# Optimization experiments

Hardware: AMD Instinct MI355X
Metric: run time of the kernel (lower is better)

Reference implementation:

```python
import jax, jax.numpy as jnp
import numpy as np

H = 128
NH = 8  # num attention heads


def _ln(x, g, b, eps=1e-5):
    m = x.mean(-1, keepdims=True)
    v = ((x - m) ** 2).mean(-1, keepdims=True)
    return (x - m) / jnp.sqrt(v + eps) * g + b


def _mha(q_in, kv_in, Wqkv, bqkv, Wo, bo):
    # torch nn.MultiheadAttention with packed in_proj, batch=1, eval (no dropout)
    h = q_in.shape[-1]
    hd = h // NH
    Wq, Wk, Wv = Wqkv[:h], Wqkv[h:2 * h], Wqkv[2 * h:]
    bq, bk, bv = bqkv[:h], bqkv[h:2 * h], bqkv[2 * h:]
    q = (q_in @ Wq.T + bq).reshape(-1, NH, hd).transpose(1, 0, 2)   # [nh, Nq, hd]
    k = (kv_in @ Wk.T + bk).reshape(-1, NH, hd).transpose(1, 0, 2)  # [nh, Nk, hd]
    v = (kv_in @ Wv.T + bv).reshape(-1, NH, hd).transpose(1, 0, 2)
    scores = jnp.einsum('hqd,hkd->hqk', q, k) / jnp.sqrt(jnp.asarray(hd, q.dtype))
    attn = jax.nn.softmax(scores, axis=-1)
    out = jnp.einsum('hqk,hkd->hqd', attn, v)                       # [nh, Nq, hd]
    out = out.transpose(1, 0, 2).reshape(-1, h)
    return out @ Wo.T + bo


def setup_inputs() -> dict:
    key = jax.random.key(0)
    ks = jax.random.split(key, 32)
    s = 0.05
    d = {
        'ligand_features': jax.random.normal(ks[0], (512, 128), jnp.float32),
        'pocket_features': jax.random.normal(ks[1], (1024, 128), jnp.float32),
        'ligand_coords': jax.random.uniform(ks[2], (512, 3), jnp.float32) * 20.0,
        'pocket_coords': jax.random.uniform(ks[3], (1024, 3), jnp.float32) * 20.0,
        # projections
        'Wl': jax.random.normal(ks[4], (H, 128), jnp.float32) * s,
        'bl': jnp.zeros((H,), jnp.float32),
        'Wp': jax.random.normal(ks[5], (H, 128), jnp.float32) * s,
        'bp': jnp.zeros((H,), jnp.float32),
        # distance encoder: 1 -> h/4 -> h/2 -> h
        'Wd1': jax.random.normal(ks[6], (H // 4, 1), jnp.float32) * s,
        'bd1': jnp.zeros((H // 4,), jnp.float32),
        'Wd2': jax.random.normal(ks[7], (H // 2, H // 4), jnp.float32) * s,
        'bd2': jnp.zeros((H // 2,), jnp.float32),
        'Wd3': jax.random.normal(ks[8], (H, H // 2), jnp.float32) * s,
        'bd3': jnp.zeros((H,), jnp.float32),
        # gates
        'Wgl': jax.random.normal(ks[9], (H, 2 * H), jnp.float32) * s,
        'bgl': jnp.zeros((H,), jnp.float32),
        'Wgp': jax.random.normal(ks[10], (H, 2 * H), jnp.float32) * s,
        'bgp': jnp.zeros((H,), jnp.float32),
        # shared cross-attention (packed qkv like torch)
        'Wqkv': jax.random.normal(ks[11], (3 * H, H), jnp.float32) * s,
        'bqkv': jnp.zeros((3 * H,), jnp.float32),
        'Wo': jax.random.normal(ks[12], (H, H), jnp.float32) * s,
        'bo': jnp.zeros((H,), jnp.float32),
        # layer norms
        'g_l': jnp.ones((H,), jnp.float32),
        'be_l': jnp.zeros((H,), jnp.float32),
        'g_p': jnp.ones((H,), jnp.float32),
        'be_p': jnp.zeros((H,), jnp.float32),
    }
    return d


def reference(ligand_features, pocket_features, ligand_coords, pocket_coords,
              Wl, bl, Wp, bp, Wd1, bd1, Wd2, bd2, Wd3, bd3,
              Wgl, bgl, Wgp, bgp, Wqkv, bqkv, Wo, bo,
              g_l, be_l, g_p, be_p):
    lig = ligand_features @ Wl.T + bl   # [Nl, H]
    poc = pocket_features @ Wp.T + bp   # [Np, H]

    # pairwise distances [Nl, Np]
    diff = ligand_coords[:, None, :] - pocket_coords[None, :, :]
    dist = jnp.sqrt(jnp.sum(diff * diff, axis=-1))

    # distance encoder MLP applied elementwise -> [Nl, Np, H]
    e = jax.nn.relu(dist[..., None] @ Wd1.T + bd1)
    e = jax.nn.relu(e @ Wd2.T + bd2)
    enc = e @ Wd3.T + bd3
    m = enc.mean(axis=-1)               # [Nl, Np]

    # ligand enhancement: softmax over pocket axis
    sw_l = jax.nn.softmax(-m, axis=-1)          # [Nl, Np]
    agg_l = sw_l @ poc                          # [Nl, H]
    gate_l = jax.nn.sigmoid(jnp.concatenate([lig, agg_l], axis=-1) @ Wgl.T + bgl)
    lig_enh = gate_l * lig + (1.0 - gate_l) * agg_l

    # pocket enhancement: transposed encoding, softmax over ligand axis
    sw_p = jax.nn.softmax(-m.T, axis=-1)        # [Np, Nl]
    agg_p = sw_p @ lig                          # [Np, H]
    gate_p = jax.nn.sigmoid(jnp.concatenate([poc, agg_p], axis=-1) @ Wgp.T + bgp)
    poc_enh = gate_p * poc + (1.0 - gate_p) * agg_p

    lig_att = _mha(lig_enh, poc_enh, Wqkv, bqkv, Wo, bo)
    poc_att = _mha(poc_enh, lig_enh, Wqkv, bqkv, Wo, bo)

    lig_fused = _ln(lig_enh + lig_att, g_l, be_l)
    poc_fused = _ln(poc_enh + poc_att, g_p, be_p)
    return (lig_fused, poc_fused)
```

## Files before the change

### kernel.cpp

```cpp
#include <hip/hip_runtime.h>
#include <math.h>

#define NL 512
#define NP 1024
#define HDIM 128

#define TAB_N 8192
#define DMAX 34.65f

#define WD3M_OFF 0
#define M_OFF    128
#define LIG_OFF  (M_OFF + NL*NP)
#define POC_OFF  (LIG_OFF + NL*HDIM)
#define LENH_OFF (POC_OFF + NP*HDIM)
#define PENH_OFF (LENH_OFF + NL*HDIM)
#define QKVL_OFF (PENH_OFF + NP*HDIM)
#define QKVP_OFF (QKVL_OFF + NL*384)
#define PARTL_OFF (QKVP_OFF + NP*384)
#define PARTP_OFF (PARTL_OFF + 512*8*8*18)
#define TAB_OFF  QKVL_OFF

__device__ __forceinline__ float dot4f(float4 a, float4 b){
  return fmaf(a.x,b.x, fmaf(a.y,b.y, fmaf(a.z,b.z, a.w*b.w)));
}

__global__ __launch_bounds__(128) void prep_kernel(const float* __restrict__ Wd3,
                                                   const float* __restrict__ bd3,
                                                   float* __restrict__ wsw){
  int t = threadIdx.x;
  if (t < 64){
    float s = 0.f;
    #pragma unroll 8
    for (int i = 0; i < 128; i++) s += Wd3[i*64 + t];
    wsw[t] = s * (1.f/128.f);
  } else if (t == 64){
    float s = 0.f;
    for (int i = 0; i < 128; i++) s += bd3[i];
    wsw[64] = s * (1.f/128.f);
  }
}

__global__ __launch_bounds__(128) void proj_kernel(const float* __restrict__ lf, const float* __restrict__ pf,
                                                   const float* __restrict__ Wl, const float* __restrict__ bl,
                                                   const float* __restrict__ Wp, const float* __restrict__ bp,
                                                   float* __restrict__ lig, float* __restrict__ poc){
  int t = threadIdx.x;
  int row0 = blockIdx.x * 4;
  const float* in; const float* W; const float* bias; float* out;
  if (row0 < NL){ in = lf + (size_t)row0*HDIM; W = Wl; bias = bl; out = lig + (size_t)row0*HDIM; }
  else { int r = row0 - NL; in = pf + (size_t)r*HDIM; W = Wp; bias = bp; out = poc + (size_t)r*HDIM; }
  __shared__ float sin[4*HDIM];
  for (int idx = t; idx < 4*HDIM; idx += 128) sin[idx] = in[idx];
  __syncthreads();
  float bv = bias[t];
  float a0 = bv, a1 = bv, a2 = bv, a3 = bv;
  const float4* wr = (const float4*)(W + (size_t)t*HDIM);
  const float4* s0 = (const float4*)(sin);
  const float4* s1 = (const float4*)(sin + HDIM);
  const float4* s2 = (const float4*)(sin + 2*HDIM);
  const float4* s3 = (const float4*)(sin + 3*HDIM);
  #pragma unroll 8
  for (int k = 0; k < 32; k++){
    float4 w = wr[k];
    a0 = fmaf(w.x, s0[k].x, fmaf(w.y, s0[k].y, fmaf(w.z, s0[k].z, fmaf(w.w, s0[k].w, a0))));
    a1 = fmaf(w.x, s1[k].x, fmaf(w.y, s1[k].y, fmaf(w.z, s1[k].z, fmaf(w.w, s1[k].w, a1))));
    a2 = fmaf(w.x, s2[k].x, fmaf(w.y, s2[k].y, fmaf(w.z, s2[k].z, fmaf(w.w, s2[k].w, a2))));
    a3 = fmaf(w.x, s3[k].x, fmaf(w.y, s3[k].y, fmaf(w.z, s3[k].z, fmaf(w.w, s3[k].w, a3))));
  }
  out[t] = a0; out[HDIM + t] = a1; out[2*HDIM + t] = a2; out[3*HDIM + t] = a3;
}

__global__ __launch_bounds__(256) void table_kernel(const float* __restrict__ Wd1, const float* __restrict__ bd1,
                                                    const float* __restrict__ Wd2, const float* __restrict__ bd2,
                                                    const float* __restrict__ wsw, float* __restrict__ tab){
  __shared__ float sWd1[32], sbd1[32], sWd2[2048], sbd2[64], swd3m[64];
  __shared__ float sbd3m;
  int t = threadIdx.x;
  int idx = blockIdx.x * 256 + t;
  if (t < 32){ sWd1[t] = Wd1[t]; sbd1[t] = bd1[t]; }
  if (t >= 32 && t < 96){ sbd2[t-32] = bd2[t-32]; swd3m[t-32] = wsw[t-32]; }
  if (t == 96) sbd3m = wsw[64];
  for (int k = t; k < 2048; k += 256) sWd2[k] = Wd2[k];
  __syncthreads();

  float d = (float)idx * (DMAX / (float)(TAB_N - 1));

  float4 e1q[8];
  const float4* w1q = (const float4*)sWd1;
  const float4* b1q = (const float4*)sbd1;
  #pragma unroll
  for (int k4 = 0; k4 < 8; k4++){
    float4 w = w1q[k4], b = b1q[k4];
    float4 e;
    e.x = fmaxf(fmaf(d, w.x, b.x), 0.f);
    e.y = fmaxf(fmaf(d, w.y, b.y), 0.f);
    e.z = fmaxf(fmaf(d, w.z, b.z), 0.f);
    e.w = fmaxf(fmaf(d, w.w, b.w), 0.f);
    e1q[k4] = e;
  }
  float mv = sbd3m;
  #pragma unroll 4
  for (int j2 = 0; j2 < 64; j2++){
    const float4* wrow = (const float4*)(sWd2 + j2*32);
    float a0 = 0.f, a1 = 0.f, a2 = 0.f, a3 = 0.f;
    #pragma unroll
    for (int k4 = 0; k4 < 8; k4++){
      float4 w = wrow[k4], e = e1q[k4];
      a0 = fmaf(w.x, e.x, a0);
      a1 = fmaf(w.y, e.y, a1);
      a2 = fmaf(w.z, e.z, a2);
      a3 = fmaf(w.w, e.w, a3);
    }
    float e2v = fmaxf(sbd2[j2] + ((a0+a1)+(a2+a3)), 0.f);
    mv = fmaf(swd3m[j2], e2v, mv);
  }
  tab[idx] = mv;
}

__global__ __launch_bounds__(1024) void agg_gate_fused(const float* __restrict__ lc, const float* __restrict__ pc,
                                                       const float* __restrict__ tab,
                                                       const float* __restrict__ lig, const float* __restrict__ poc,
                                                       const float* __restrict__ Wgl, const float* __restrict__ bgl,
                                                       const float* __restrict__ Wgp, const float* __restrict__ bgp,
                                                       float* __restrict__ lenh, float* __restrict__ penh){
  int r = blockIdx.x, t = threadIdx.x;
  __shared__ float stab[TAB_N];
  __shared__ float w[NP];
  __shared__ float red[20];
  __shared__ float part[4096];
  __shared__ float sx[HDIM], sa[HDIM];
  __shared__ float gpart[512];
  bool isLig = (r < NL);
  int n = isLig ? NP : NL;
  int rloc = isLig ? r : (r - NL);

  for (int k = t; k < TAB_N/4; k += 1024) ((float4*)stab)[k] = ((const float4*)tab)[k];

  const float* ccoord = isLig ? (lc + rloc*3) : (pc + rloc*3);
  float cx = ccoord[0], cy = ccoord[1], cz = ccoord[2];
  bool active = t < n;
  float ox = 0.f, oy = 0.f, oz = 0.f;
  if (active){
    const float* oc = isLig ? (pc + t*3) : (lc + t*3);
    ox = oc[0]; oy = oc[1]; oz = oc[2];
  }
  if (t < HDIM) sx[t] = isLig ? lig[(size_t)rloc*HDIM + t] : poc[(size_t)rloc*HDIM + t];
  __syncthreads();

  float x = -1e30f;
  if (active){
    float dx = cx-ox, dy = cy-oy, dz = cz-oz;
    float d = sqrtf(fmaf(dx,dx, fmaf(dy,dy, dz*dz)));
    float xf = d * ((float)(TAB_N-1)/DMAX);
    int i0 = (int)xf;
    i0 = (i0 > TAB_N-2) ? (TAB_N-2) : i0;
    float f = xf - (float)i0;
    float v0 = stab[i0], v1 = stab[i0+1];
    x = -fmaf(f, v1 - v0, v0);
  }

  float v = x;
  #pragma unroll
  for (int off = 32; off; off >>= 1) v = fmaxf(v, __shfl_down(v, off));
  int wid = t >> 6, lane = t & 63;
  if (lane == 0) red[wid] = v;
  __syncthreads();
  if (t == 0){ float mm = red[0]; for (int k = 1; k < 16; k++) mm = fmaxf(mm, red[k]); red[16] = mm; }
  __syncthreads();
  float mx = red[16];

  float e = active ? __expf(x - mx) : 0.f;
  w[t] = e;
  v = e;
  #pragma unroll
  for (int off = 32; off; off >>= 1) v += __shfl_down(v, off);
  if (lane == 0) red[wid] = v;
  __syncthreads();
  if (t == 0){ float ss = 0.f; for (int k = 0; k < 16; k++) ss += red[k]; red[17] = 1.0f / ss; }
  __syncthreads();
  float inv = red[17];

  int jg = t >> 5, c4 = t & 31;
  int per = n >> 5;
  const float4* src4 = (const float4*)(isLig ? poc : lig);
  int j0 = jg * per;
  float4 acc = {0.f, 0.f, 0.f, 0.f};
  #pragma unroll 4
  for (int jj = 0; jj < per; jj++){
    int j = j0 + jj;
    float wj = w[j];
    float4 sv = src4[(size_t)j*32 + c4];
    acc.x = fmaf(wj, sv.x, acc.x);
    acc.y = fmaf(wj, sv.y, acc.y);
    acc.z = fmaf(wj, sv.z, acc.z);
    acc.w = fmaf(wj, sv.w, acc.w);
  }
  float4* p4 = (float4*)part;
  p4[jg*32 + c4] = acc;
  __syncthreads();
  #pragma unroll
  for (int s = 16; s >= 1; s >>= 1){
    if (jg < s){
      float4 a = p4[jg*32 + c4], b = p4[(jg+s)*32 + c4];
      a.x += b.x; a.y += b.y; a.z += b.z; a.w += b.w;
      p4[jg*32 + c4] = a;
    }
    __syncthreads();
  }
  if (t < 32){
    float4 a = p4[t];
    sa[t*4+0] = a.x*inv; sa[t*4+1] = a.y*inv; sa[t*4+2] = a.z*inv; sa[t*4+3] = a.w*inv;
  }
  __syncthreads();

  if (t < 512){
    int col = t & 127, qg = t >> 7;
    const float* Wg = isLig ? Wgl : Wgp;
    const float4* wr = (const float4*)(Wg + (size_t)col*256 + qg*64);
    const float4* inq = (qg < 2) ? ((const float4*)sx + qg*16) : ((const float4*)sa + (qg-2)*16);
    float g = 0.f;
    #pragma unroll
    for (int k = 0; k < 16; k++) g += dot4f(wr[k], inq[k]);
    gpart[qg*128 + col] = g;
  }
  __syncthreads();
  if (t < 128){
    const float* bg = isLig ? bgl : bgp;
    float g = bg[t] + ((gpart[t] + gpart[128+t]) + (gpart[256+t] + gpart[384+t]));
    g = 1.0f / (1.0f + __expf(-g));
    float* dst = isLig ? (lenh + (size_t)rloc*HDIM) : (penh + (size_t)rloc*HDIM);
    dst[t] = fmaf(g, sx[t] - sa[t], sa[t]);
  }
}

__global__ __launch_bounds__(384) void qkv_kernel(const float* __restrict__ lenh, const float* __restrict__ penh,
                                                  const float* __restrict__ Wqkv, const float* __restrict__ bqkv,
                                                  float* __restrict__ qkvl, float* __restrict__ qkvp){
  int t = threadIdx.x;
  int row0 = blockIdx.x * 4;
  const float* in; float* out; int rloc;
  if (row0 < NL){ in = lenh + (size_t)row0*HDIM; out = qkvl; rloc = row0; }
  else { rloc = row0 - NL; in = penh + (size_t)rloc*HDIM; out = qkvp; }
  __shared__ float sin[4*HDIM];
  for (int idx = t; idx < 4*HDIM; idx += 384) sin[idx] = in[idx];
  __syncthreads();
  float bv = bqkv[t];
  float a0 = bv, a1 = bv, a2 = bv, a3 = bv;
  const float4* wr = (const float4*)(Wqkv + (size_t)t*HDIM);
  const float4* s0 = (const float4*)(sin);
  const float4* s1 = (const float4*)(sin + HDIM);
  const float4* s2 = (const float4*)(sin + 2*HDIM);
  const float4* s3 = (const float4*)(sin + 3*HDIM);
  #pragma unroll 8
  for (int k = 0; k < 32; k++){
    float4 w = wr[k];
    a0 = fmaf(w.x, s0[k].x, fmaf(w.y, s0[k].y, fmaf(w.z, s0[k].z, fmaf(w.w, s0[k].w, a0))));
    a1 = fmaf(w.x, s1[k].x, fmaf(w.y, s1[k].y, fmaf(w.z, s1[k].z, fmaf(w.w, s1[k].w, a1))));
    a2 = fmaf(w.x, s2[k].x, fmaf(w.y, s2[k].y, fmaf(w.z, s2[k].z, fmaf(w.w, s2[k].w, a2))));
    a3 = fmaf(w.x, s3[k].x, fmaf(w.y, s3[k].y, fmaf(w.z, s3[k].z, fmaf(w.w, s3[k].w, a3))));
  }
  out[(size_t)(rloc+0)*384 + t] = a0;
  out[(size_t)(rloc+1)*384 + t] = a1;
  out[(size_t)(rloc+2)*384 + t] = a2;
  out[(size_t)(rloc+3)*384 + t] = a3;
}

__global__ __launch_bounds__(256) void attn_part(const float* __restrict__ qkvl, const float* __restrict__ qkvp,
                                                 float* __restrict__ partL, float* __restrict__ partP){
  int bx = blockIdx.x;
  int t = threadIdx.x;
  const float* qsrc; const float* kvsrc; int qt, slice; bool isLig;
  if (bx < 256){ isLig = true;  qt = bx >> 3; slice = bx & 7; qsrc = qkvl; kvsrc = qkvp; }
  else { int b2 = bx - 256; isLig = false; qt = b2 >> 2; slice = b2 & 3; qsrc = qkvp; kvsrc = qkvl; }
  int g = t >> 7, tt = t & 127;
  int h = tt >> 4, q = tt & 15;
  int j0 = slice*128 + g*64;

  const float4* qp = (const float4*)(qsrc + (size_t)(qt*16+q)*384 + h*16);
  float4 q0 = qp[0], q1 = qp[1], q2 = qp[2], q3 = qp[3];
  float m = -1e30f, l = 0.f;
  float4 O0 = {0,0,0,0}, O1 = {0,0,0,0}, O2 = {0,0,0,0}, O3 = {0,0,0,0};

  __shared__ float sKV[8192];
  float* myKV = sKV + g*4096;

  for (int tile = 0; tile < 4; tile++){
    int jbase = j0 + tile*16;
    __syncthreads();
    #pragma unroll
    for (int n = 0; n < 8; n++){
      int v4 = tt + n*128;
      int jj = v4 >> 6, c4 = v4 & 63;
      ((float4*)myKV)[(size_t)jj*64 + c4] = *(const float4*)(kvsrc + (size_t)(jbase+jj)*384 + 128 + c4*4);
    }
    __syncthreads();
    float s[16];
    #pragma unroll
    for (int jj = 0; jj < 16; jj++){
      const float4* kk = (const float4*)(myKV + jj*256 + h*16);
      s[jj] = (dot4f(q0, kk[0]) + dot4f(q1, kk[1]) + dot4f(q2, kk[2]) + dot4f(q3, kk[3])) * 0.25f;
    }
    float mt = s[0];
    #pragma unroll
    for (int jj = 1; jj < 16; jj++) mt = fmaxf(mt, s[jj]);
    float mn = fmaxf(m, mt);
    float corr = __expf(m - mn);
    l *= corr;
    O0.x*=corr; O0.y*=corr; O0.z*=corr; O0.w*=corr;
    O1.x*=corr; O1.y*=corr; O1.z*=corr; O1.w*=corr;
    O2.x*=corr; O2.y*=corr; O2.z*=corr; O2.w*=corr;
    O3.x*=corr; O3.y*=corr; O3.z*=corr; O3.w*=corr;
    #pragma unroll
    for (int jj = 0; jj < 16; jj++){
      float p = __expf(s[jj] - mn);
      l += p;
      const float4* vv = (const float4*)(myKV + jj*256 + 128 + h*16);
      O0.x = fmaf(p, vv[0].x, O0.x); O0.y = fmaf(p, vv[0].y, O0.y);
      O0.z = fmaf(p, vv[0].z, O0.z); O0.w = fmaf(p, vv[0].w, O0.w);
      O1.x = fmaf(p, vv[1].x, O1.x); O1.y = fmaf(p, vv[1].y, O1.y);
      O1.z = fmaf(p, vv[1].z, O1.z); O1.w = fmaf(p, vv[1].w, O1.w);
      O2.x = fmaf(p, vv[2].x, O2.x); O2.y = fmaf(p, vv[2].y, O2.y);
      O2.z = fmaf(p, vv[2].z, O2.z); O2.w = fmaf(p, vv[2].w, O2.w);
      O3.x = fmaf(p, vv[3].x, O3.x); O3.y = fmaf(p, vv[3].y, O3.y);
      O3.z = fmaf(p, vv[3].z, O3.z); O3.w = fmaf(p, vv[3].w, O3.w);
    }
    m = mn;
  }

  __syncthreads();
  float* smerge = sKV;
  if (g == 1){
    float* b = smerge + tt*19;
    b[0] = m; b[1] = l;
    b[2]=O0.x; b[3]=O0.y; b[4]=O0.z; b[5]=O0.w;
    b[6]=O1.x; b[7]=O1.y; b[8]=O1.z; b[9]=O1.w;
    b[10]=O2.x; b[11]=O2.y; b[12]=O2.z; b[13]=O2.w;
    b[14]=O3.x; b[15]=O3.y; b[16]=O3.z; b[17]=O3.w;
  }
  __syncthreads();
  if (g == 0){
    const float* b = smerge + tt*19;
    float m1 = b[0], l1 = b[1];
    float M = fmaxf(m, m1);
    float e0 = __expf(m - M), e1 = __expf(m1 - M);
    float L = l*e0 + l1*e1;
    float* dst;
    if (isLig) dst = partL + ((size_t)((qt*16+q)*8 + h)*8 + slice)*18;
    else       dst = partP + ((size_t)((qt*16+q)*8 + h)*4 + slice)*18;
    dst[0] = M; dst[1] = L;
    dst[2]  = O0.x*e0 + b[2]*e1;  dst[3]  = O0.y*e0 + b[3]*e1;
    dst[4]  = O0.z*e0 + b[4]*e1;  dst[5]  = O0.w*e0 + b[5]*e1;
    dst[6]  = O1.x*e0 + b[6]*e1;  dst[7]  = O1.y*e0 + b[7]*e1;
    dst[8]  = O1.z*e0 + b[8]*e1;  dst[9]  = O1.w*e0 + b[9]*e1;
    dst[10] = O2.x*e0 + b[10]*e1; dst[11] = O2.y*e0 + b[11]*e1;
    dst[12] = O2.z*e0 + b[12]*e1; dst[13] = O2.w*e0 + b[13]*e1;
    dst[14] = O3.x*e0 + b[14]*e1; dst[15] = O3.y*e0 + b[15]*e1;
    dst[16] = O3.z*e0 + b[16]*e1; dst[17] = O3.w*e0 + b[17]*e1;
  }
}

__global__ __launch_bounds__(128) void merge_ln(const float* __restrict__ partL, const float* __restrict__ partP,
                                                const float* __restrict__ lenh, const float* __restrict__ penh,
                                                const float* __restrict__ Wo, const float* __restrict__ bo,
                                                const float* __restrict__ g_l, const float* __restrict__ be_l,
                                                const float* __restrict__ g_p, const float* __restrict__ be_p,
                                                float* __restrict__ out){
  int r = blockIdx.x, t = threadIdx.x;
  int h = t >> 4, c = t & 15;
  int ns; const float* base;
  if (r < NL){ ns = 8; base = partL + ((size_t)(r*8 + h))*8*18; }
  else       { ns = 4; base = partP + ((size_t)((r-NL)*8 + h))*4*18; }
  float M = -1e30f;
  for (int s = 0; s < ns; s++) M = fmaxf(M, base[s*18]);
  float Lsum = 0.f, Osum = 0.f;
  for (int s = 0; s < ns; s++){
    float e = __expf(base[s*18] - M);
    Lsum = fmaf(e, base[s*18+1], Lsum);
    Osum = fmaf(e, base[s*18+2+c], Osum);
  }
  __shared__ float satt[HDIM];
  satt[t] = Osum / Lsum;
  __syncthreads();
  float o = bo[t];
  const float4* wr = (const float4*)(Wo + (size_t)t*HDIM);
  const float4* sv = (const float4*)satt;
  #pragma unroll 8
  for (int k = 0; k < 32; k++) o += dot4f(wr[k], sv[k]);
  const float* enh = (r < NL) ? (lenh + (size_t)r*HDIM) : (penh + (size_t)(r-NL)*HDIM);
  float x = enh[t] + o;
  __shared__ float red[HDIM];
  red[t] = x; __syncthreads();
  #pragma unroll
  for (int s = 64; s > 0; s >>= 1){ if (t < s) red[t] += red[t+s]; __syncthreads(); }
  float mu = red[0] * (1.f/128.f); __syncthreads();
  float dx = x - mu;
  red[t] = dx*dx; __syncthreads();
  #pragma unroll
  for (int s = 64; s > 0; s >>= 1){ if (t < s) red[t] += red[t+s]; __syncthreads(); }
  float var = red[0] * (1.f/128.f);
  float y = dx * rsqrtf(var + 1e-5f);
  if (r < NL){
    y = fmaf(y, g_l[t], be_l[t]);
    out[(size_t)r*HDIM + t] = y;
  } else {
    y = fmaf(y, g_p[t], be_p[t]);
    out[(size_t)NL*HDIM + (size_t)(r-NL)*HDIM + t] = y;
  }
}

extern "C" void kernel_launch(void* const* d_in, const int* in_sizes, int n_in,
                              void* d_out, int out_size, void* d_ws, size_t ws_size,
                              hipStream_t stream){
  const float* lf   = (const float*)d_in[0];
  const float* pf   = (const float*)d_in[1];
  const float* lc   = (const float*)d_in[2];
  const float* pc   = (const float*)d_in[3];
  const float* Wl   = (const float*)d_in[4];
  const float* bl   = (const float*)d_in[5];
  const float* Wp   = (const float*)d_in[6];
  const float* bp   = (const float*)d_in[7];
  const float* Wd1  = (const float*)d_in[8];
  const float* bd1  = (const float*)d_in[9];
  const float* Wd2  = (const float*)d_in[10];
  const float* bd2  = (const float*)d_in[11];
  const float* Wd3  = (const float*)d_in[12];
  const float* bd3  = (const float*)d_in[13];
  const float* Wgl  = (const float*)d_in[14];
  const float* bgl  = (const float*)d_in[15];
  const float* Wgp  = (const float*)d_in[16];
  const float* bgp  = (const float*)d_in[17];
  const float* Wqkv = (const float*)d_in[18];
  const float* bqkv = (const float*)d_in[19];
  const float* Wo   = (const float*)d_in[20];
  const float* bo   = (const float*)d_in[21];
  const float* g_l  = (const float*)d_in[22];
  const float* be_l = (const float*)d_in[23];
  const float* g_p  = (const float*)d_in[24];
  const float* be_p = (const float*)d_in[25];

  float* ws  = (float*)d_ws;
  float* out = (float*)d_out;
  float* wsw   = ws + WD3M_OFF;
  float* lig   = ws + LIG_OFF;
  float* poc   = ws + POC_OFF;
  float* lenh  = ws + LENH_OFF;
  float* penh  = ws + PENH_OFF;
  float* qkvl  = ws + QKVL_OFF;
  float* qkvp  = ws + QKVP_OFF;
  float* partL = ws + PARTL_OFF;
  float* partP = ws + PARTP_OFF;
  float* tab   = ws + TAB_OFF;

  prep_kernel<<<1, 128, 0, stream>>>(Wd3, bd3, wsw);
  table_kernel<<<TAB_N/256, 256, 0, stream>>>(Wd1, bd1, Wd2, bd2, wsw, tab);
  proj_kernel<<<384, 128, 0, stream>>>(lf, pf, Wl, bl, Wp, bp, lig, poc);
  agg_gate_fused<<<NL + NP, 1024, 0, stream>>>(lc, pc, tab, lig, poc, Wgl, bgl, Wgp, bgp, lenh, penh);
  qkv_kernel<<<384, 384, 0, stream>>>(lenh, penh, Wqkv, bqkv, qkvl, qkvp);
  attn_part<<<512, 256, 0, stream>>>(qkvl, qkvp, partL, partP);
  merge_ln<<<1536, 128, 0, stream>>>(partL, partP, lenh, penh, Wo, bo, g_l, be_l, g_p, be_p, out);
}
```

Baseline: 233.4 us.

## Process four rows per block in aggregation-gate kernel and drop shared table copy

```diff
diff --git a/kernel.cpp b/kernel.cpp
--- a/kernel.cpp
+++ b/kernel.cpp
@@ -123,113 +123,122 @@
                                                        const float* __restrict__ Wgl, const float* __restrict__ bgl,
                                                        const float* __restrict__ Wgp, const float* __restrict__ bgp,
                                                        float* __restrict__ lenh, float* __restrict__ penh){
-  int r = blockIdx.x, t = threadIdx.x;
-  __shared__ float stab[TAB_N];
-  __shared__ float w[NP];
-  __shared__ float red[20];
-  __shared__ float part[4096];
-  __shared__ float sx[HDIM], sa[HDIM];
-  __shared__ float gpart[512];
-  bool isLig = (r < NL);
+  int b = blockIdx.x, t = threadIdx.x;
+  bool isLig = (b < NL/4);
+  int r0 = isLig ? b*4 : (b - NL/4)*4;
   int n = isLig ? NP : NL;
-  int rloc = isLig ? r : (r - NL);
-
-  for (int k = t; k < TAB_N/4; k += 1024) ((float4*)stab)[k] = ((const float4*)tab)[k];
-
-  const float* ccoord = isLig ? (lc + rloc*3) : (pc + rloc*3);
-  float cx = ccoord[0], cy = ccoord[1], cz = ccoord[2];
-  bool active = t < n;
-  float ox = 0.f, oy = 0.f, oz = 0.f;
-  if (active){
-    const float* oc = isLig ? (pc + t*3) : (lc + t*3);
-    ox = oc[0]; oy = oc[1]; oz = oc[2];
-  }
-  if (t < HDIM) sx[t] = isLig ? lig[(size_t)rloc*HDIM + t] : poc[(size_t)rloc*HDIM + t];
-  __syncthreads();
-
-  float x = -1e30f;
-  if (active){
+  const float* myFeat = isLig ? lig : poc;
+  const float* otherFeat = isLig ? poc : lig;
+  const float* myC = isLig ? lc : pc;
+  const float* otC = isLig ? pc : lc;
+
+  __shared__ float w[4*NP];
+  __shared__ float sx[4*HDIM];
+  __shared__ float sa[4*HDIM];
+  __shared__ float part[8*512];
+  __shared__ float gpart[4*2*128];
+  __shared__ float redm[16];
+  __shared__ float sgm[4], sinv[4];
+
+  int rr = t >> 8, u = t & 255;
+  int lane = t & 63, wv = t >> 6;
+  int row = r0 + rr;
+
+  if (t < 512) sx[t] = myFeat[(size_t)r0*HDIM + t];
+
+  float cx = myC[row*3+0], cy = myC[row*3+1], cz = myC[row*3+2];
+  const float inv_h = (float)(TAB_N - 1) / DMAX;
+  int per = n >> 8;
+
+  float xs[4];
+  float lmax = -1e30f;
+  for (int k = 0; k < per; k++){
+    int j = u + (k << 8);
+    float ox = otC[j*3+0], oy = otC[j*3+1], oz = otC[j*3+2];
     float dx = cx-ox, dy = cy-oy, dz = cz-oz;
     float d = sqrtf(fmaf(dx,dx, fmaf(dy,dy, dz*dz)));
-    float xf = d * ((float)(TAB_N-1)/DMAX);
+    float xf = d * inv_h;
     int i0 = (int)xf;
     i0 = (i0 > TAB_N-2) ? (TAB_N-2) : i0;
     float f = xf - (float)i0;
-    float v0 = stab[i0], v1 = stab[i0+1];
-    x = -fmaf(f, v1 - v0, v0);
-  }
-
-  float v = x;
+    float v0 = tab[i0], v1 = tab[i0+1];
+    xs[k] = -fmaf(f, v1 - v0, v0);
+    lmax = fmaxf(lmax, xs[k]);
+  }
+  float v = lmax;
   #pragma unroll
   for (int off = 32; off; off >>= 1) v = fmaxf(v, __shfl_down(v, off));
-  int wid = t >> 6, lane = t & 63;
-  if (lane == 0) red[wid] = v;
-  __syncthreads();
-  if (t == 0){ float mm = red[0]; for (int k = 1; k < 16; k++) mm = fmaxf(mm, red[k]); red[16] = mm; }
-  __syncthreads();
-  float mx = red[16];
-
-  float e = active ? __expf(x - mx) : 0.f;
-  w[t] = e;
-  v = e;
+  if (lane == 0) redm[wv] = v;
+  __syncthreads();
+  if (t < 4) sgm[t] = fmaxf(fmaxf(redm[t*4+0], redm[t*4+1]), fmaxf(redm[t*4+2], redm[t*4+3]));
+  __syncthreads();
+  float gm = sgm[rr];
+  float lsum = 0.f;
+  for (int k = 0; k < per; k++){
+    float e = __expf(xs[k] - gm);
+    w[rr*NP + u + (k << 8)] = e;
+    lsum += e;
+  }
+  v = lsum;
   #pragma unroll
   for (int off = 32; off; off >>= 1) v += __shfl_down(v, off);
-  if (lane == 0) red[wid] = v;
-  __syncthreads();
-  if (t == 0){ float ss = 0.f; for (int k = 0; k < 16; k++) ss += red[k]; red[17] = 1.0f / ss; }
-  __syncthreads();
-  float inv = red[17];
-
-  int jg = t >> 5, c4 = t & 31;
-  int per = n >> 5;
-  const float4* src4 = (const float4*)(isLig ? poc : lig);
-  int j0 = jg * per;
-  float4 acc = {0.f, 0.f, 0.f, 0.f};
-  #pragma unroll 4
-  for (int jj = 0; jj < per; jj++){
-    int j = j0 + jj;
-    float wj = w[j];
-    float4 sv = src4[(size_t)j*32 + c4];
-    acc.x = fmaf(wj, sv.x, acc.x);
-    acc.y = fmaf(wj, sv.y, acc.y);
-    acc.z = fmaf(wj, sv.z, acc.z);
-    acc.w = fmaf(wj, sv.w, acc.w);
-  }
-  float4* p4 = (float4*)part;
-  p4[jg*32 + c4] = acc;
-  __syncthreads();
-  #pragma unroll
-  for (int s = 16; s >= 1; s >>= 1){
-    if (jg < s){
-      float4 a = p4[jg*32 + c4], b = p4[(jg+s)*32 + c4];
-      a.x += b.x; a.y += b.y; a.z += b.z; a.w += b.w;
-      p4[jg*32 + c4] = a;
+  if (lane == 0) redm[wv] = v;
+  __syncthreads();
+  if (t < 4) sinv[t] = 1.0f / ((redm[t*4+0] + redm[t*4+1]) + (redm[t*4+2] + redm[t*4+3]));
+  __syncthreads();
+
+  {
+    int jg = t >> 7, cc = t & 127;
+    int per2 = n >> 3;
+    int jb0 = jg * per2;
+    float a0 = 0.f, a1 = 0.f, a2 = 0.f, a3 = 0.f;
+    #pragma unroll 4
+    for (int jj = 0; jj < per2; jj++){
+      int j = jb0 + jj;
+      float f = otherFeat[(size_t)j*HDIM + cc];
+      a0 = fmaf(w[j], f, a0);
+      a1 = fmaf(w[NP + j], f, a1);
+      a2 = fmaf(w[2*NP + j], f, a2);
+      a3 = fmaf(w[3*NP + j], f, a3);
     }
+    part[jg*512 + 0*128 + cc] = a0;
+    part[jg*512 + 1*128 + cc] = a1;
+    part[jg*512 + 2*128 + cc] = a2;
+    part[jg*512 + 3*128 + cc] = a3;
+  }
+  __syncthreads();
+  #pragma unroll
+  for (int s = 4; s >= 1; s >>= 1){
+    for (int e = t; e < s*512; e += 1024) part[e] += part[e + s*512];
     __syncthreads();
   }
-  if (t < 32){
-    float4 a = p4[t];
-    sa[t*4+0] = a.x*inv; sa[t*4+1] = a.y*inv; sa[t*4+2] = a.z*inv; sa[t*4+3] = a.w*inv;
-  }
-  __syncthreads();
-
   if (t < 512){
-    int col = t & 127, qg = t >> 7;
+    int r = t >> 7;
+    sa[t] = part[t] * sinv[r];
+  }
+  __syncthreads();
+
+  {
+    int r = t >> 8;
+    int kg = (t >> 7) & 1;
+    int col = t & 127;
     const float* Wg = isLig ? Wgl : Wgp;
-    const float4* wr = (const float4*)(Wg + (size_t)col*256 + qg*64);
-    const float4* inq = (qg < 2) ? ((const float4*)sx + qg*16) : ((const float4*)sa + (qg-2)*16);
+    const float4* wr = (const float4*)(Wg + (size_t)col*256 + kg*128);
+    const float4* inq = (kg == 0) ? (const float4*)(sx + r*128) : (const float4*)(sa + r*128);
     float g = 0.f;
-    #pragma unroll
-    for (int k = 0; k < 16; k++) g += dot4f(wr[k], inq[k]);
-    gpart[qg*128 + col] = g;
-  }
-  __syncthreads();
-  if (t < 128){
+    #pragma unroll 8
+    for (int k = 0; k < 32; k++) g += dot4f(wr[k], inq[k]);
+    gpart[r*256 + kg*128 + col] = g;
+  }
+  __syncthreads();
+  if (t < 512){
+    int r = t >> 7, c = t & 127;
     const float* bg = isLig ? bgl : bgp;
-    float g = bg[t] + ((gpart[t] + gpart[128+t]) + (gpart[256+t] + gpart[384+t]));
+    float g = bg[c] + gpart[r*256 + c] + gpart[r*256 + 128 + c];
     g = 1.0f / (1.0f + __expf(-g));
-    float* dst = isLig ? (lenh + (size_t)rloc*HDIM) : (penh + (size_t)rloc*HDIM);
-    dst[t] = fmaf(g, sx[t] - sa[t], sa[t]);
+    float xv = sx[r*128 + c], av = sa[r*128 + c];
+    float* dst = isLig ? (lenh + (size_t)(r0+r)*HDIM) : (penh + (size_t)(r0+r)*HDIM);
+    dst[c] = fmaf(g, xv - av, av);
   }
 }
 
@@ -454,7 +463,7 @@
   prep_kernel<<<1, 128, 0, stream>>>(Wd3, bd3, wsw);
   table_kernel<<<TAB_N/256, 256, 0, stream>>>(Wd1, bd1, Wd2, bd2, wsw, tab);
   proj_kernel<<<384, 128, 0, stream>>>(lf, pf, Wl, bl, Wp, bp, lig, poc);
-  agg_gate_fused<<<NL + NP, 1024, 0, stream>>>(lc, pc, tab, lig, poc, Wgl, bgl, Wgp, bgp, lenh, penh);
+  agg_gate_fused<<<NL/4 + NP/4, 1024, 0, stream>>>(lc, pc, tab, lig, poc, Wgl, bgl, Wgp, bgp, lenh, penh);
   qkv_kernel<<<384, 384, 0, stream>>>(lenh, penh, Wqkv, bqkv, qkvl, qkvp);
   attn_part<<<512, 256, 0, stream>>>(qkvl, qkvp, partL, partP);
   merge_ln<<<1536, 128, 0, stream>>>(partL, partP, lenh, penh, Wo, bo, g_l, be_l, g_p, be_p, out);
```

Measured after the change: 232.7 us. No clear change (-0.3%).
